# Kernel optimization log

Hardware: AMD Instinct MI355X
Metric: run time of the kernel (lower is better)

The kernel has to match this reference:

```python
import jax, jax.numpy as jnp
import numpy as np

RATIO, NH, NG, KS, RF, UP = 4, 2, 2, 3, 11.0, 2


def _cln(t, g, b):
    # channel-wise LayerNorm on NCHW (LayerNormProxy), eps=1e-5
    mu = t.mean(axis=1, keepdims=True)
    var = ((t - mu) ** 2).mean(axis=1, keepdims=True)
    return (t - mu) * jax.lax.rsqrt(var + 1e-5) * g[None, :, None, None] + b[None, :, None, None]


def _resize_ac(img, oH, oW):
    # bilinear resize, align_corners=True (F.interpolate)
    H, W = img.shape[-2], img.shape[-1]
    ys = jnp.arange(oH, dtype=img.dtype) * ((H - 1) / (oH - 1))
    y0 = jnp.clip(jnp.floor(ys), 0, H - 2).astype(jnp.int32)
    wy = ys - y0.astype(img.dtype)
    xs = jnp.arange(oW, dtype=img.dtype) * ((W - 1) / (oW - 1))
    x0 = jnp.clip(jnp.floor(xs), 0, W - 2).astype(jnp.int32)
    wx = xs - x0.astype(img.dtype)
    t = img[..., y0, :] * (1.0 - wy)[:, None] + img[..., y0 + 1, :] * wy[:, None]
    return t[..., x0] * (1.0 - wx) + t[..., x0 + 1] * wx


def _grid_sample(img, iy, ix):
    # bilinear grid_sample, padding_mode='zeros', align_corners=True
    # img [Bg,Cx,H,W]; iy,ix [Bg,N] unnormalized input-pixel coords
    H, W = img.shape[-2], img.shape[-1]
    def one(im, yy, xx):
        y0f, x0f = jnp.floor(yy), jnp.floor(xx)
        wy, wx = yy - y0f, xx - x0f
        y0, x0 = y0f.astype(jnp.int32), x0f.astype(jnp.int32)
        def gat(yi, xi):
            valid = ((yi >= 0) & (yi < H) & (xi >= 0) & (xi < W)).astype(im.dtype)
            return im[:, jnp.clip(yi, 0, H - 1), jnp.clip(xi, 0, W - 1)] * valid[None]
        return (gat(y0, x0) * ((1 - wy) * (1 - wx))[None]
                + gat(y0, x0 + 1) * ((1 - wy) * wx)[None]
                + gat(y0 + 1, x0) * (wy * (1 - wx))[None]
                + gat(y0 + 1, x0 + 1) * (wy * wx)[None])
    return jax.vmap(one)(img, iy, ix)


def _conv2d(x, w, groups=1):
    return jax.lax.conv_general_dilated(x, w, (1, 1), 'SAME', feature_group_count=groups,
                                        dimension_numbers=('NCHW', 'OIHW', 'NCHW'))


def _forward(x, ln_g, ln_b, Wq, Wk, dw_w, off_ln_g, off_ln_b, off_w, off_b, rpb):
    B, C, H, W = x.shape
    hidden = C // RATIO
    gc = hidden // NG
    c2 = hidden // NH          # attn_dim per head
    oH, oW = int(H * UP), int(W * UP)
    N1, n = oH * oW, KS * KS
    scale = c2 ** -0.5
    v = x
    xn = _cln(x, ln_g, ln_b)
    q = jnp.einsum('oc,bchw->bohw', Wq, xn)
    k = jnp.einsum('oc,bchw->bohw', Wk, xn)
    q = _resize_ac(q, oH, oW)                        # [B,hidden,oH,oW]
    # offset prediction
    q_off = q.reshape(B * NG, gc, oH, oW)
    t = _conv2d(q_off, dw_w, groups=gc)
    t = _cln(t, off_ln_g, off_ln_b)
    t = jax.nn.gelu(t, approximate=False)
    pred = _conv2d(t, off_w) + off_b[None, :, None, None]  # [Bg,2*ks^2,oH,oW]
    pad = (KS - 1) // 2
    rng = jnp.arange(-pad, pad + 1, dtype=x.dtype)
    base = jnp.stack(jnp.meshgrid(rng, rng, indexing='ij'), axis=-1)  # [KS,KS,2] (y,x)
    off = jnp.tanh(pred).reshape(B * NG, KS, KS, 2, oH, oW) * RF + base[None, :, :, :, None, None]
    py = off[:, :, :, 0] + jnp.arange(oH, dtype=x.dtype)[None, None, None, :, None]
    px = off[:, :, :, 1] + jnp.arange(oW, dtype=x.dtype)[None, None, None, None, :]
    # normalize over (oH-1,oW-1) then denormalize onto (H-1,W-1) input grid (align_corners)
    iy = (py * ((H - 1) / (oH - 1))).reshape(B * NG, -1)
    ix = (px * ((W - 1) / (oW - 1))).reshape(B * NG, -1)
    kg = k.reshape(B * NG, hidden // NG, H, W)
    vg = v.reshape(B * NG, C // NG, H, W)
    kf = _grid_sample(kg, iy, ix).reshape(B, NG, hidden // NG, n, oH, oW)
    vf = _grid_sample(vg, iy, ix).reshape(B, NG, C // NG, n, oH, oW)
    # -> [B, N1, n, g*c] -> [B, nh, N1, n, c]
    kf = kf.transpose(0, 4, 5, 3, 1, 2).reshape(B, N1, n, NH, hidden // NH).transpose(0, 3, 1, 2, 4)
    vf = vf.transpose(0, 4, 5, 3, 1, 2).reshape(B, N1, n, NH, C // NH).transpose(0, 3, 1, 2, 4)
    kf = kf + rpb                                     # relative position bias on K
    qh = q.reshape(B, NH, c2, N1).transpose(0, 1, 3, 2) * scale  # [B,nh,N1,c2]
    attn = jax.nn.softmax(jnp.einsum('bhnc,bhnkc->bhnk', qh, kf), axis=-1)
    out = jnp.einsum('bhnk,bhnkc->bhnc', attn, vf)    # [B,nh,N1,C/nh]
    return out.transpose(0, 1, 3, 2).reshape(B, C, oH, oW)


def setup_inputs() -> dict:
    key = jax.random.key(0)
    ks = jax.random.split(key, 8)
    B, C, H, W = 2, 256, 48, 48
    hidden = C // RATIO
    gc = hidden // NG
    c2 = hidden // NH
    f32 = jnp.float32
    return {
        'x': jax.random.normal(ks[0], (B, C, H, W), f32),
        'ln_g': jnp.ones((C,), f32),
        'ln_b': jnp.zeros((C,), f32),
        'Wq': jax.random.normal(ks[1], (hidden, C), f32) * 0.05,
        'Wk': jax.random.normal(ks[2], (hidden, C), f32) * 0.05,
        'dw_w': jax.random.normal(ks[3], (gc, 1, 3, 3), f32) * 0.1,
        'off_ln_g': jnp.ones((gc,), f32),
        'off_ln_b': jnp.zeros((gc,), f32),
        'off_w': jax.random.normal(ks[4], (2 * KS * KS, gc, 3, 3), f32) * 0.02,
        'off_b': jnp.zeros((2 * KS * KS,), f32),
        'rpb': jax.random.normal(ks[5], (1, NH, 1, KS * KS, c2), f32) * 0.02,
    }


def reference(x, ln_g, ln_b, Wq, Wk, dw_w, off_ln_g, off_ln_b, off_w, off_b, rpb):
    return _forward(x, ln_g, ln_b, Wq, Wk, dw_w, off_ln_g, off_ln_b, off_w, off_b, rpb)
```

## Files before the change

kernel.cpp:

```cpp
#include <hip/hip_runtime.h>
#include <cstdint>
#include <cmath>

#define NB 2
#define NC 256
#define HW 2304
#define HID 64
#define OH 96
#define OW 96
#define N1 9216
#define SCALE_ATTN 0.17677669529663689f
#define RESZ ((float)(47.0/95.0))

__device__ __host__ inline int ocb_of(int w) { return w < 2 ? w * 5 : 10 + (w - 2) * 4; }
__device__ __host__ inline int cnt_of(int w) { return w < 2 ? 5 : 4; }

__global__ void kA_prep(const float* __restrict__ x, const float* __restrict__ Wq,
                        const float* __restrict__ Wk, const float* __restrict__ off_w,
                        const float* __restrict__ dw_w, const float* __restrict__ off_b,
                        float* __restrict__ v_nhwc, float* __restrict__ WT4,
                        float* __restrict__ dwT, float* __restrict__ wg,
                        float* __restrict__ bsg) {
    int blk = blockIdx.x;
    if (blk < 1152) {
        int pt = blk % 72;
        int t2 = blk / 72;
        int ct = t2 & 3;
        int bg = t2 >> 2;
        int b = bg >> 1, g = bg & 1;
        __shared__ float tile[32][33];
        int tx = threadIdx.x & 31, row = threadIdx.x >> 5;
#pragma unroll
        for (int r = 0; r < 4; r++) {
            int c = ct * 32 + row + r * 8;
            tile[row + r * 8][tx] = x[((size_t)(b * 256 + g * 128 + c)) * HW + pt * 32 + tx];
        }
        __syncthreads();
#pragma unroll
        for (int r = 0; r < 4; r++) {
            int p = pt * 32 + row + r * 8;
            v_nhwc[((size_t)bg * HW + p) * 128 + ct * 32 + tx] = tile[tx][row + r * 8];
        }
    } else {
        int idx = (blk - 1152) * 256 + threadIdx.x;
        if (idx < 256 * 128) {
            int c = idx >> 7, t = idx & 127;
            float v = (t < 64) ? Wq[t * 256 + c] : Wk[(t - 64) * 256 + c];
            WT4[(((size_t)(c >> 2) * 128) + t) * 4 + (c & 3)] = v;
        } else if (idx < 256 * 128 + 288) {
            int i = idx - 256 * 128;
            int wi = i >> 5, c = i & 31;
            dwT[i] = dw_w[c * 9 + wi];
        } else if (idx < 256 * 128 + 288 + 4 * 288 * 5) {
            int i = idx - (256 * 128 + 288);
            int w = i / 1440, r = i - w * 1440;
            int kk = r / 5, j = r - kk * 5;
            wg[i] = (j < cnt_of(w)) ? off_w[(ocb_of(w) + j) * 288 + kk] : 0.f;
        } else if (idx < 256 * 128 + 288 + 4 * 288 * 5 + 20) {
            int i = idx - (256 * 128 + 288 + 4 * 288 * 5);
            int w = i / 5, j = i - w * 5;
            bsg[i] = (j < cnt_of(w)) ? off_b[ocb_of(w) + j] : 0.f;
        }
    }
}

__global__ __launch_bounds__(256) void k1_ln_qk(const float* __restrict__ v_nhwc,
                         const float* __restrict__ ln_g, const float* __restrict__ ln_b,
                         const float* __restrict__ WT4,
                         float* __restrict__ q_pix, float* __restrict__ k_nhwc) {
    int blk = blockIdx.x;
    int tid = threadIdx.x;
    int wv = tid >> 6, lane = tid & 63;
    __shared__ float xs[4][256];
    {
        int pix = blk * 4 + wv;
        int b = pix / HW, p = pix - b * HW;
        int c0 = lane * 2;
        float2 u0 = *(const float2*)(v_nhwc + (((size_t)(b * 2 + 0) * HW) + p) * 128 + c0);
        float2 u1 = *(const float2*)(v_nhwc + (((size_t)(b * 2 + 1) * HW) + p) * 128 + c0);
        float s = u0.x + u0.y + u1.x + u1.y;
#pragma unroll
        for (int off = 1; off < 64; off <<= 1) s += __shfl_xor(s, off);
        float mu = s * (1.f / 256.f);
        float d0 = u0.x - mu, d1 = u0.y - mu, d2 = u1.x - mu, d3 = u1.y - mu;
        float q = d0 * d0 + d1 * d1 + d2 * d2 + d3 * d3;
#pragma unroll
        for (int off = 1; off < 64; off <<= 1) q += __shfl_xor(q, off);
        float rs = rsqrtf(q * (1.f / 256.f) + 1e-5f);
        float2 w0, w1;
        w0.x = d0 * rs * ln_g[c0] + ln_b[c0];
        w0.y = d1 * rs * ln_g[c0 + 1] + ln_b[c0 + 1];
        w1.x = d2 * rs * ln_g[128 + c0] + ln_b[128 + c0];
        w1.y = d3 * rs * ln_g[129 + c0] + ln_b[129 + c0];
        *(float2*)&xs[wv][c0] = w0;
        *(float2*)&xs[wv][128 + c0] = w1;
    }
    __syncthreads();
    int o = tid & 127, ph = tid >> 7;
    float a0 = 0.f, a1 = 0.f;
    const float4* wp = (const float4*)WT4 + o;
    const float4* xa = (const float4*)xs[ph * 2];
    const float4* xb4 = (const float4*)xs[ph * 2 + 1];
#pragma unroll 8
    for (int c4 = 0; c4 < 64; c4++) {
        float4 w = wp[(size_t)c4 * 128];
        float4 p0 = xa[c4], p1 = xb4[c4];
        a0 += w.x * p0.x + w.y * p0.y + w.z * p0.z + w.w * p0.w;
        a1 += w.x * p1.x + w.y * p1.y + w.z * p1.z + w.w * p1.w;
    }
#pragma unroll
    for (int k = 0; k < 2; k++) {
        int pix = blk * 4 + ph * 2 + k;
        int b = pix / HW, p = pix - b * HW;
        float a = k ? a1 : a0;
        if (o < 64) {
            q_pix[(((size_t)b * HW) + p) * 64 + o] = a;
        } else {
            int t = o - 64, g = t >> 5, c32 = t & 31;
            k_nhwc[(((size_t)(b * 2 + g) * HW) + p) * 32 + c32] = a;
        }
    }
}

__global__ __launch_bounds__(256) void k34_off(const float* __restrict__ q_pix,
                                               const float* __restrict__ dwT,
                                               const float* __restrict__ og,
                                               const float* __restrict__ ob,
                                               const float* __restrict__ wg,
                                               const float* __restrict__ bsg,
                                               float* __restrict__ pred) {
    int blk = blockIdx.x;
    int bg = blk / 144, tile = blk - bg * 144;
    int ty0 = (tile / 12) * 8, tx0 = (tile % 12) * 8;
    int b = bg >> 1, g = bg & 1;
    int tid = threadIdx.x;
    __shared__ float ts[100 * 33];

    const float* qb = q_pix + ((size_t)b * HW) * 64 + g * 32;
    for (int item = tid; item < 3200; item += 256) {
        int pt = item >> 5, c = item & 31;
        int pyh = pt / 10, pxh = pt - pyh * 10;
        int hy = ty0 + pyh - 1, hx = tx0 + pxh - 1;
        bool inb = ((unsigned)hy < (unsigned)OH) && ((unsigned)hx < (unsigned)OW);
        float acc = 0.f;
        if (inb) {
#pragma unroll
            for (int dy = -1; dy <= 1; dy++) {
                int yy = hy + dy;
                if ((unsigned)yy >= (unsigned)OH) continue;
                float ysf = yy * RESZ;
                int y0 = min((int)ysf, 46);
                float wy = ysf - (float)y0;
#pragma unroll
                for (int dx = -1; dx <= 1; dx++) {
                    int xx = hx + dx;
                    if ((unsigned)xx >= (unsigned)OW) continue;
                    float xsf = xx * RESZ;
                    int x0 = min((int)xsf, 46);
                    float wx = xsf - (float)x0;
                    int i00 = (y0 * 48 + x0) * 64;
                    float q00 = qb[i00 + c], q01 = qb[i00 + 64 + c];
                    float q10 = qb[i00 + 48 * 64 + c], q11 = qb[i00 + 49 * 64 + c];
                    float qv = (q00 * (1.f - wy) + q10 * wy) * (1.f - wx)
                             + (q01 * (1.f - wy) + q11 * wy) * wx;
                    acc += qv * dwT[((dy + 1) * 3 + dx + 1) * 32 + c];
                }
            }
        }
        float s = acc;
#pragma unroll
        for (int off = 1; off < 32; off <<= 1) s += __shfl_xor(s, off);
        float mu = s * (1.f / 32.f);
        float d = acc - mu;
        float v = d * d;
#pragma unroll
        for (int off = 1; off < 32; off <<= 1) v += __shfl_xor(v, off);
        float rsv = rsqrtf(v * (1.f / 32.f) + 1e-5f);
        float t = d * rsv * og[c] + ob[c];
        float ge = 0.5f * t * (1.f + erff(t * 0.70710678118654752f));
        ts[pt * 33 + c] = inb ? ge : 0.f;
    }
    __syncthreads();

    int w = __builtin_amdgcn_readfirstlane(tid >> 6);
    int lane = tid & 63;
    int y = lane >> 3, x = lane & 7;
    int ocb = ocb_of(w), cnt = cnt_of(w);
    float acc[5];
#pragma unroll
    for (int j = 0; j < 5; j++) acc[j] = bsg[w * 5 + j];
    const float* tsb = &ts[(y * 10 + x) * 33];
    const float* wgp = wg + (size_t)w * 1440;
    const int kof[9] = {0, 33, 66, 330, 363, 396, 660, 693, 726};
    for (int ic = 0; ic < 32; ic++) {
#pragma unroll
        for (int k = 0; k < 9; k++) {
            float tv = tsb[kof[k] + ic];
            const float* wr = wgp + (ic * 9 + k) * 5;
#pragma unroll
            for (int j = 0; j < 5; j++) acc[j] += tv * wr[j];
        }
    }
    int p = (ty0 + y) * OW + tx0 + x;
    float* pp = pred + ((size_t)bg * N1 + p) * 18 + ocb;
#pragma unroll
    for (int j = 0; j < 5; j++)
        if (j < cnt) pp[j] = acc[j];
}

__global__ __launch_bounds__(256) void k5_attn(const float* __restrict__ pred,
                                               const float* __restrict__ q_pix,
                                               const float* __restrict__ k_nhwc,
                                               const float* __restrict__ v_nhwc,
                                               const float* __restrict__ rpb,
                                               float* __restrict__ out) {
    int tid = threadIdx.x;
    int wv = __builtin_amdgcn_readfirstlane(tid >> 6);
    int lane = tid & 63;
    int gp = blockIdx.x * 16;
    int bg = gp / N1, p0 = gp % N1;
    int b = bg >> 1, g = bg & 1;
    int pw = p0 + wv * 4;
    int oy = pw / OW, ox0 = pw % OW;

    __shared__ float4 wts[4][4][9];
    __shared__ int4   cof[4][4][9];
    __shared__ float  outb[4][4][128];

    if (lane < 36) {
        int px = lane / 9, j = lane % 9;
        int p = pw + px;
        int ky = j / 3, kx = j % 3;
        const float* pp = pred + ((size_t)bg * N1 + p) * 18;
        float pr0 = pp[j * 2];
        float pr1 = pp[j * 2 + 1];
        float th0 = 1.f - 2.f * __builtin_amdgcn_rcpf(__expf(2.f * pr0) + 1.f);
        float th1 = 1.f - 2.f * __builtin_amdgcn_rcpf(__expf(2.f * pr1) + 1.f);
        float py  = th0 * 11.0f + (float)(ky - 1) + (float)oy;
        float pxc = th1 * 11.0f + (float)(kx - 1) + (float)(ox0 + px);
        float iy = py * RESZ, ix = pxc * RESZ;
        float y0f = floorf(iy), x0f = floorf(ix);
        float wy = iy - y0f, wx = ix - x0f;
        int y0 = (int)y0f, x0 = (int)x0f;
        bool vy0 = (unsigned)y0 < 48u, vy1 = (unsigned)(y0 + 1) < 48u;
        bool vx0 = (unsigned)x0 < 48u, vx1 = (unsigned)(x0 + 1) < 48u;
        int y0c = min(max(y0, 0), 47), y1c = min(max(y0 + 1, 0), 47);
        int x0c = min(max(x0, 0), 47), x1c = min(max(x0 + 1, 0), 47);
        float4 w;
        w.x = (vy0 && vx0) ? (1.f - wy) * (1.f - wx) : 0.f;
        w.y = (vy0 && vx1) ? (1.f - wy) * wx : 0.f;
        w.z = (vy1 && vx0) ? wy * (1.f - wx) : 0.f;
        w.w = (vy1 && vx1) ? wy * wx : 0.f;
        wts[wv][px][j] = w;
        cof[wv][px][j] = make_int4(y0c * 48 + x0c, y0c * 48 + x1c,
                                   y1c * 48 + x0c, y1c * 48 + x1c);
    }
    __syncthreads();

    int c = lane & 31, h = lane >> 5;
    int c4 = (lane & 31) * 4;
    const float* kb = k_nhwc + (size_t)bg * HW * 32;
    const float* rb = rpb + (size_t)g * 288;
    const float* qb = q_pix + (size_t)b * HW * 64 + g * 32 + c;
    const float* vbase = v_nhwc + (size_t)bg * HW * 128;

    float ysf = oy * RESZ;
    int qy0 = min((int)ysf, 46);
    float qwy = ysf - (float)qy0;

    for (int px = 0; px < 4; px++) {
        float xsf = (ox0 + px) * RESZ;
        int qx0 = min((int)xsf, 46);
        float qwx = xsf - (float)qx0;
        int qi = (qy0 * 48 + qx0) * 64;
        float q00 = qb[qi], q01 = qb[qi + 64];
        float q10 = qb[qi + 48 * 64], q11 = qb[qi + 49 * 64];
        float qv = ((q00 * (1.f - qwy) + q10 * qwy) * (1.f - qwx)
                  + (q01 * (1.f - qwy) + q11 * qwy) * qwx) * SCALE_ATTN;

        float s[5], e[5];
#pragma unroll
        for (int jj = 0; jj < 5; jj++) {
            int j = jj * 2 + h;
            float partial = 0.f;
            if (j < 9) {
                float4 w = wts[wv][px][j];
                int4 co = cof[wv][px][j];
                float kv = w.x * kb[co.x * 32 + c] + w.y * kb[co.y * 32 + c]
                         + w.z * kb[co.z * 32 + c] + w.w * kb[co.w * 32 + c];
                partial = qv * (kv + rb[j * 32 + c]);
            }
#pragma unroll
            for (int off = 1; off < 32; off <<= 1) partial += __shfl_xor(partial, off);
            s[jj] = (j < 9) ? partial : -1e30f;
        }
        float m = s[0];
#pragma unroll
        for (int jj = 1; jj < 5; jj++) m = fmaxf(m, s[jj]);
        m = fmaxf(m, __shfl_xor(m, 32));
        float sum = 0.f;
#pragma unroll
        for (int jj = 0; jj < 5; jj++) { e[jj] = __expf(s[jj] - m); sum += e[jj]; }
        sum += __shfl_xor(sum, 32);
        float inv = __builtin_amdgcn_rcpf(sum);

        float4 acc = make_float4(0.f, 0.f, 0.f, 0.f);
#pragma unroll
        for (int jj = 0; jj < 5; jj++) {
            int j = jj * 2 + h;
            if (j < 9) {
                float pj = e[jj] * inv;
                float4 w = wts[wv][px][j];
                int4 co = cof[wv][px][j];
                float4 a0 = *(const float4*)(vbase + (size_t)co.x * 128 + c4);
                float4 a1 = *(const float4*)(vbase + (size_t)co.y * 128 + c4);
                float4 a2 = *(const float4*)(vbase + (size_t)co.z * 128 + c4);
                float4 a3 = *(const float4*)(vbase + (size_t)co.w * 128 + c4);
                float f0 = w.x * pj, f1 = w.y * pj, f2 = w.z * pj, f3 = w.w * pj;
                acc.x += f0 * a0.x + f1 * a1.x + f2 * a2.x + f3 * a3.x;
                acc.y += f0 * a0.y + f1 * a1.y + f2 * a2.y + f3 * a3.y;
                acc.z += f0 * a0.z + f1 * a1.z + f2 * a2.z + f3 * a3.z;
                acc.w += f0 * a0.w + f1 * a1.w + f2 * a2.w + f3 * a3.w;
            }
        }
        acc.x += __shfl_xor(acc.x, 32);
        acc.y += __shfl_xor(acc.y, 32);
        acc.z += __shfl_xor(acc.z, 32);
        acc.w += __shfl_xor(acc.w, 32);
        if (lane < 32) *(float4*)&outb[wv][px][c4] = acc;
    }
    __syncthreads();

    if (tid < 128) {
        int ch = tid;
        float* op = out + ((size_t)b * NC + g * 128 + ch) * N1 + p0;
#pragma unroll
        for (int w2 = 0; w2 < 4; w2++) {
            float4 v4 = make_float4(outb[w2][0][ch], outb[w2][1][ch],
                                    outb[w2][2][ch], outb[w2][3][ch]);
            *(float4*)(op + w2 * 4) = v4;
        }
    }
}

extern "C" void kernel_launch(void* const* d_in, const int* in_sizes, int n_in,
                              void* d_out, int out_size, void* d_ws, size_t ws_size,
                              hipStream_t stream) {
    const float* x      = (const float*)d_in[0];
    const float* ln_g   = (const float*)d_in[1];
    const float* ln_b   = (const float*)d_in[2];
    const float* Wq     = (const float*)d_in[3];
    const float* Wk     = (const float*)d_in[4];
    const float* dw_w   = (const float*)d_in[5];
    const float* off_g  = (const float*)d_in[6];
    const float* off_bt = (const float*)d_in[7];
    const float* off_w  = (const float*)d_in[8];
    const float* off_b  = (const float*)d_in[9];
    const float* rpb    = (const float*)d_in[10];
    float* out = (float*)d_out;

    float* ws = (float*)d_ws;
    float* v_nhwc = ws;
    float* WT4    = v_nhwc + 1179648;
    float* k_nhwc = WT4 + 32768;
    float* q_pix  = k_nhwc + 294912;
    float* pred   = q_pix + 294912;
    float* dwT    = pred + 663552;
    float* wg     = dwT + 288;
    float* bsg    = wg + 5760;

    kA_prep<<<1304, 256, 0, stream>>>(x, Wq, Wk, off_w, dw_w, off_b,
                                      v_nhwc, WT4, dwT, wg, bsg);
    k1_ln_qk<<<1152, 256, 0, stream>>>(v_nhwc, ln_g, ln_b, WT4, q_pix, k_nhwc);
    k34_off<<<576, 256, 0, stream>>>(q_pix, dwT, off_g, off_bt, wg, bsg, pred);
    k5_attn<<<2304, 256, 0, stream>>>(pred, q_pix, k_nhwc, v_nhwc, rpb, out);
}
```

Measured before the change: 185.1 us.

## Split offset kernel into depthwise-LN-GELU pass with fp16 buffer and 8-wave conv

The fused offset kernel used to recompute the depthwise conv, LayerNorm and GELU for every halo pixel of each 8x8 tile. It is now split into a per-pixel kernel that writes the activations once to an fp16 buffer, and a conv kernel that loads halo tiles from that buffer using 512 threads, so each wave handles 2-3 output channels. The attention kernel is also restructured to batch the q interpolation, score, softmax and value accumulation across its 4 pixels, which exposes more independent loads. This adds an extra launch and fp16 rounding of intermediate activations, and it raises register pressure in the attention kernel.

```diff
diff --git a/kernel.cpp b/kernel.cpp
--- a/kernel.cpp
+++ b/kernel.cpp
@@ -1,4 +1,5 @@
 #include <hip/hip_runtime.h>
+#include <hip/hip_fp16.h>
 #include <cstdint>
 #include <cmath>
 
@@ -12,15 +13,15 @@
 #define SCALE_ATTN 0.17677669529663689f
 #define RESZ ((float)(47.0/95.0))
 
-__device__ __host__ inline int ocb_of(int w) { return w < 2 ? w * 5 : 10 + (w - 2) * 4; }
-__device__ __host__ inline int cnt_of(int w) { return w < 2 ? 5 : 4; }
+__device__ __host__ inline int ocb8(int w) { return w < 2 ? 3 * w : 6 + 2 * (w - 2); }
+__device__ __host__ inline int cnt8(int w) { return w < 2 ? 3 : 2; }
 
 __global__ void kA_prep(const float* __restrict__ x, const float* __restrict__ Wq,
                         const float* __restrict__ Wk, const float* __restrict__ off_w,
                         const float* __restrict__ dw_w, const float* __restrict__ off_b,
                         float* __restrict__ v_nhwc, float* __restrict__ WT4,
-                        float* __restrict__ dwT, float* __restrict__ wg,
-                        float* __restrict__ bsg) {
+                        float* __restrict__ dwT, float* __restrict__ wg2,
+                        float* __restrict__ bsg2) {
     int blk = blockIdx.x;
     if (blk < 1152) {
         int pt = blk % 72;
@@ -43,23 +44,23 @@
         }
     } else {
         int idx = (blk - 1152) * 256 + threadIdx.x;
-        if (idx < 256 * 128) {
+        if (idx < 32768) {
             int c = idx >> 7, t = idx & 127;
             float v = (t < 64) ? Wq[t * 256 + c] : Wk[(t - 64) * 256 + c];
             WT4[(((size_t)(c >> 2) * 128) + t) * 4 + (c & 3)] = v;
-        } else if (idx < 256 * 128 + 288) {
-            int i = idx - 256 * 128;
+        } else if (idx < 32768 + 288) {
+            int i = idx - 32768;
             int wi = i >> 5, c = i & 31;
             dwT[i] = dw_w[c * 9 + wi];
-        } else if (idx < 256 * 128 + 288 + 4 * 288 * 5) {
-            int i = idx - (256 * 128 + 288);
-            int w = i / 1440, r = i - w * 1440;
-            int kk = r / 5, j = r - kk * 5;
-            wg[i] = (j < cnt_of(w)) ? off_w[(ocb_of(w) + j) * 288 + kk] : 0.f;
-        } else if (idx < 256 * 128 + 288 + 4 * 288 * 5 + 20) {
-            int i = idx - (256 * 128 + 288 + 4 * 288 * 5);
-            int w = i / 5, j = i - w * 5;
-            bsg[i] = (j < cnt_of(w)) ? off_b[ocb_of(w) + j] : 0.f;
+        } else if (idx < 32768 + 288 + 8 * 288 * 3) {
+            int i = idx - (32768 + 288);
+            int w = i / 864, r = i - w * 864;
+            int kk = r / 3, j = r - kk * 3;
+            wg2[i] = (j < cnt8(w)) ? off_w[(ocb8(w) + j) * 288 + kk] : 0.f;
+        } else if (idx < 32768 + 288 + 8 * 288 * 3 + 24) {
+            int i = idx - (32768 + 288 + 8 * 288 * 3);
+            int w = i / 3, j = i - w * 3;
+            bsg2[i] = (j < cnt8(w)) ? off_b[ocb8(w) + j] : 0.f;
         }
     }
 }
@@ -122,89 +123,107 @@
     }
 }
 
-__global__ __launch_bounds__(256) void k34_off(const float* __restrict__ q_pix,
-                                               const float* __restrict__ dwT,
-                                               const float* __restrict__ og,
-                                               const float* __restrict__ ob,
-                                               const float* __restrict__ wg,
-                                               const float* __restrict__ bsg,
+__global__ __launch_bounds__(256) void k3_t(const float* __restrict__ q_pix,
+                                            const float* __restrict__ dwT,
+                                            const float* __restrict__ og,
+                                            const float* __restrict__ ob,
+                                            __half* __restrict__ tbuf_h) {
+    int gid = blockIdx.x * 256 + threadIdx.x;
+    int c = gid & 31;
+    int p2 = gid >> 5;
+    int bg = p2 / N1, p = p2 - bg * N1;
+    int b = bg >> 1, g = bg & 1;
+    int oy = p / OW, ox = p - oy * OW;
+    const float* qb = q_pix + ((size_t)b * HW) * 64 + g * 32 + c;
+    float acc = 0.f;
+#pragma unroll
+    for (int dy = -1; dy <= 1; dy++) {
+        int yy = oy + dy;
+        if ((unsigned)yy >= (unsigned)OH) continue;
+        float ysf = yy * RESZ;
+        int y0 = min((int)ysf, 46);
+        float wy = ysf - (float)y0;
+#pragma unroll
+        for (int dx = -1; dx <= 1; dx++) {
+            int xx = ox + dx;
+            if ((unsigned)xx >= (unsigned)OW) continue;
+            float xsf = xx * RESZ;
+            int x0 = min((int)xsf, 46);
+            float wx = xsf - (float)x0;
+            int i00 = (y0 * 48 + x0) * 64;
+            float q00 = qb[i00], q01 = qb[i00 + 64];
+            float q10 = qb[i00 + 48 * 64], q11 = qb[i00 + 49 * 64];
+            float qv = (q00 * (1.f - wy) + q10 * wy) * (1.f - wx)
+                     + (q01 * (1.f - wy) + q11 * wy) * wx;
+            acc += qv * dwT[((dy + 1) * 3 + dx + 1) * 32 + c];
+        }
+    }
+    float s = acc;
+#pragma unroll
+    for (int off = 1; off < 32; off <<= 1) s += __shfl_xor(s, off);
+    float mu = s * (1.f / 32.f);
+    float d = acc - mu;
+    float v = d * d;
+#pragma unroll
+    for (int off = 1; off < 32; off <<= 1) v += __shfl_xor(v, off);
+    float rsv = rsqrtf(v * (1.f / 32.f) + 1e-5f);
+    float t = d * rsv * og[c] + ob[c];
+    float ge = 0.5f * t * (1.f + erff(t * 0.70710678118654752f));
+    tbuf_h[(size_t)p2 * 32 + c] = __float2half(ge);
+}
+
+__global__ __launch_bounds__(512) void k4_pred(const __half* __restrict__ tbuf_h,
+                                               const float* __restrict__ wg2,
+                                               const float* __restrict__ bsg2,
                                                float* __restrict__ pred) {
     int blk = blockIdx.x;
     int bg = blk / 144, tile = blk - bg * 144;
     int ty0 = (tile / 12) * 8, tx0 = (tile % 12) * 8;
-    int b = bg >> 1, g = bg & 1;
     int tid = threadIdx.x;
     __shared__ float ts[100 * 33];
 
-    const float* qb = q_pix + ((size_t)b * HW) * 64 + g * 32;
-    for (int item = tid; item < 3200; item += 256) {
-        int pt = item >> 5, c = item & 31;
-        int pyh = pt / 10, pxh = pt - pyh * 10;
-        int hy = ty0 + pyh - 1, hx = tx0 + pxh - 1;
-        bool inb = ((unsigned)hy < (unsigned)OH) && ((unsigned)hx < (unsigned)OW);
-        float acc = 0.f;
-        if (inb) {
-#pragma unroll
-            for (int dy = -1; dy <= 1; dy++) {
-                int yy = hy + dy;
-                if ((unsigned)yy >= (unsigned)OH) continue;
-                float ysf = yy * RESZ;
-                int y0 = min((int)ysf, 46);
-                float wy = ysf - (float)y0;
-#pragma unroll
-                for (int dx = -1; dx <= 1; dx++) {
-                    int xx = hx + dx;
-                    if ((unsigned)xx >= (unsigned)OW) continue;
-                    float xsf = xx * RESZ;
-                    int x0 = min((int)xsf, 46);
-                    float wx = xsf - (float)x0;
-                    int i00 = (y0 * 48 + x0) * 64;
-                    float q00 = qb[i00 + c], q01 = qb[i00 + 64 + c];
-                    float q10 = qb[i00 + 48 * 64 + c], q11 = qb[i00 + 49 * 64 + c];
-                    float qv = (q00 * (1.f - wy) + q10 * wy) * (1.f - wx)
-                             + (q01 * (1.f - wy) + q11 * wy) * wx;
-                    acc += qv * dwT[((dy + 1) * 3 + dx + 1) * 32 + c];
-                }
-            }
-        }
-        float s = acc;
-#pragma unroll
-        for (int off = 1; off < 32; off <<= 1) s += __shfl_xor(s, off);
-        float mu = s * (1.f / 32.f);
-        float d = acc - mu;
-        float v = d * d;
-#pragma unroll
-        for (int off = 1; off < 32; off <<= 1) v += __shfl_xor(v, off);
-        float rsv = rsqrtf(v * (1.f / 32.f) + 1e-5f);
-        float t = d * rsv * og[c] + ob[c];
-        float ge = 0.5f * t * (1.f + erff(t * 0.70710678118654752f));
-        ts[pt * 33 + c] = inb ? ge : 0.f;
+    const __half* tb = tbuf_h + (size_t)bg * N1 * 32;
+    for (int item = tid; item < 400; item += 512) {
+        int pt = item >> 2, qg = item & 3;
+        int hy = ty0 + pt / 10 - 1;
+        int hx = tx0 + pt % 10 - 1;
+        float4 raw = make_float4(0.f, 0.f, 0.f, 0.f);
+        if ((unsigned)hy < (unsigned)OH && (unsigned)hx < (unsigned)OW)
+            raw = *(const float4*)(tb + ((size_t)(hy * OW + hx)) * 32 + qg * 8);
+        const __half2* h2 = (const __half2*)&raw;
+        int base = pt * 33 + qg * 8;
+#pragma unroll
+        for (int i = 0; i < 4; i++) {
+            float2 f = __half22float2(h2[i]);
+            ts[base + i * 2] = f.x;
+            ts[base + i * 2 + 1] = f.y;
+        }
     }
     __syncthreads();
 
     int w = __builtin_amdgcn_readfirstlane(tid >> 6);
     int lane = tid & 63;
     int y = lane >> 3, x = lane & 7;
-    int ocb = ocb_of(w), cnt = cnt_of(w);
-    float acc[5];
-#pragma unroll
-    for (int j = 0; j < 5; j++) acc[j] = bsg[w * 5 + j];
+    int ocb = ocb8(w), cnt = cnt8(w);
+    float acc[3];
+#pragma unroll
+    for (int j = 0; j < 3; j++) acc[j] = bsg2[w * 3 + j];
     const float* tsb = &ts[(y * 10 + x) * 33];
-    const float* wgp = wg + (size_t)w * 1440;
+    const float* wgp = wg2 + (size_t)w * 864;
     const int kof[9] = {0, 33, 66, 330, 363, 396, 660, 693, 726};
     for (int ic = 0; ic < 32; ic++) {
 #pragma unroll
         for (int k = 0; k < 9; k++) {
             float tv = tsb[kof[k] + ic];
-            const float* wr = wgp + (ic * 9 + k) * 5;
-#pragma unroll
-            for (int j = 0; j < 5; j++) acc[j] += tv * wr[j];
+            const float* wr = wgp + (ic * 9 + k) * 3;
+#pragma unroll
+            for (int j = 0; j < 3; j++) acc[j] += tv * wr[j];
         }
     }
     int p = (ty0 + y) * OW + tx0 + x;
     float* pp = pred + ((size_t)bg * N1 + p) * 18 + ocb;
 #pragma unroll
-    for (int j = 0; j < 5; j++)
+    for (int j = 0; j < 3; j++)
         if (j < cnt) pp[j] = acc[j];
 }
 
@@ -268,6 +287,15 @@
     int qy0 = min((int)ysf, 46);
     float qwy = ysf - (float)qy0;
 
+    float rv[5];
+#pragma unroll
+    for (int jj = 0; jj < 5; jj++) {
+        int j = jj * 2 + h;
+        rv[jj] = (j < 9) ? rb[j * 32 + c] : 0.f;
+    }
+
+    float qv[4];
+#pragma unroll
     for (int px = 0; px < 4; px++) {
         float xsf = (ox0 + px) * RESZ;
         int qx0 = min((int)xsf, 46);
@@ -275,10 +303,13 @@
         int qi = (qy0 * 48 + qx0) * 64;
         float q00 = qb[qi], q01 = qb[qi + 64];
         float q10 = qb[qi + 48 * 64], q11 = qb[qi + 49 * 64];
-        float qv = ((q00 * (1.f - qwy) + q10 * qwy) * (1.f - qwx)
-                  + (q01 * (1.f - qwy) + q11 * qwy) * qwx) * SCALE_ATTN;
-
-        float s[5], e[5];
+        qv[px] = ((q00 * (1.f - qwy) + q10 * qwy) * (1.f - qwx)
+                + (q01 * (1.f - qwy) + q11 * qwy) * qwx) * SCALE_ATTN;
+    }
+
+    float s[4][5];
+#pragma unroll
+    for (int px = 0; px < 4; px++) {
 #pragma unroll
         for (int jj = 0; jj < 5; jj++) {
             int j = jj * 2 + h;
@@ -288,28 +319,40 @@
                 int4 co = cof[wv][px][j];
                 float kv = w.x * kb[co.x * 32 + c] + w.y * kb[co.y * 32 + c]
                          + w.z * kb[co.z * 32 + c] + w.w * kb[co.w * 32 + c];
-                partial = qv * (kv + rb[j * 32 + c]);
+                partial = qv[px] * (kv + rv[jj]);
             }
 #pragma unroll
             for (int off = 1; off < 32; off <<= 1) partial += __shfl_xor(partial, off);
-            s[jj] = (j < 9) ? partial : -1e30f;
-        }
-        float m = s[0];
-#pragma unroll
-        for (int jj = 1; jj < 5; jj++) m = fmaxf(m, s[jj]);
+            s[px][jj] = (j < 9) ? partial : -1e30f;
+        }
+    }
+
+#pragma unroll
+    for (int px = 0; px < 4; px++) {
+        float m = s[px][0];
+#pragma unroll
+        for (int jj = 1; jj < 5; jj++) m = fmaxf(m, s[px][jj]);
         m = fmaxf(m, __shfl_xor(m, 32));
+        float e[5];
         float sum = 0.f;
 #pragma unroll
-        for (int jj = 0; jj < 5; jj++) { e[jj] = __expf(s[jj] - m); sum += e[jj]; }
+        for (int jj = 0; jj < 5; jj++) { e[jj] = __expf(s[px][jj] - m); sum += e[jj]; }
         sum += __shfl_xor(sum, 32);
         float inv = __builtin_amdgcn_rcpf(sum);
-
-        float4 acc = make_float4(0.f, 0.f, 0.f, 0.f);
+#pragma unroll
+        for (int jj = 0; jj < 5; jj++) s[px][jj] = e[jj] * inv;
+    }
+
+    float4 acc[4];
+#pragma unroll
+    for (int px = 0; px < 4; px++) acc[px] = make_float4(0.f, 0.f, 0.f, 0.f);
+#pragma unroll
+    for (int px = 0; px < 4; px++) {
 #pragma unroll
         for (int jj = 0; jj < 5; jj++) {
             int j = jj * 2 + h;
             if (j < 9) {
-                float pj = e[jj] * inv;
+                float pj = s[px][jj];
                 float4 w = wts[wv][px][j];
                 int4 co = cof[wv][px][j];
                 float4 a0 = *(const float4*)(vbase + (size_t)co.x * 128 + c4);
@@ -317,17 +360,20 @@
                 float4 a2 = *(const float4*)(vbase + (size_t)co.z * 128 + c4);
                 float4 a3 = *(const float4*)(vbase + (size_t)co.w * 128 + c4);
                 float f0 = w.x * pj, f1 = w.y * pj, f2 = w.z * pj, f3 = w.w * pj;
-                acc.x += f0 * a0.x + f1 * a1.x + f2 * a2.x + f3 * a3.x;
-                acc.y += f0 * a0.y + f1 * a1.y + f2 * a2.y + f3 * a3.y;
-                acc.z += f0 * a0.z + f1 * a1.z + f2 * a2.z + f3 * a3.z;
-                acc.w += f0 * a0.w + f1 * a1.w + f2 * a2.w + f3 * a3.w;
+                acc[px].x += f0 * a0.x + f1 * a1.x + f2 * a2.x + f3 * a3.x;
+                acc[px].y += f0 * a0.y + f1 * a1.y + f2 * a2.y + f3 * a3.y;
+                acc[px].z += f0 * a0.z + f1 * a1.z + f2 * a2.z + f3 * a3.z;
+                acc[px].w += f0 * a0.w + f1 * a1.w + f2 * a2.w + f3 * a3.w;
             }
         }
-        acc.x += __shfl_xor(acc.x, 32);
-        acc.y += __shfl_xor(acc.y, 32);
-        acc.z += __shfl_xor(acc.z, 32);
-        acc.w += __shfl_xor(acc.w, 32);
-        if (lane < 32) *(float4*)&outb[wv][px][c4] = acc;
+    }
+#pragma unroll
+    for (int px = 0; px < 4; px++) {
+        acc[px].x += __shfl_xor(acc[px].x, 32);
+        acc[px].y += __shfl_xor(acc[px].y, 32);
+        acc[px].z += __shfl_xor(acc[px].z, 32);
+        acc[px].w += __shfl_xor(acc[px].w, 32);
+        if (lane < 32) *(float4*)&outb[wv][px][c4] = acc[px];
     }
     __syncthreads();
 
@@ -366,12 +412,14 @@
     float* q_pix  = k_nhwc + 294912;
     float* pred   = q_pix + 294912;
     float* dwT    = pred + 663552;
-    float* wg     = dwT + 288;
-    float* bsg    = wg + 5760;
-
-    kA_prep<<<1304, 256, 0, stream>>>(x, Wq, Wk, off_w, dw_w, off_b,
-                                      v_nhwc, WT4, dwT, wg, bsg);
+    float* wg2    = dwT + 288;
+    float* bsg2   = wg2 + 6912;
+    __half* tbuf_h = (__half*)(bsg2 + 24);
+
+    kA_prep<<<1309, 256, 0, stream>>>(x, Wq, Wk, off_w, dw_w, off_b,
+                                      v_nhwc, WT4, dwT, wg2, bsg2);
     k1_ln_qk<<<1152, 256, 0, stream>>>(v_nhwc, ln_g, ln_b, WT4, q_pix, k_nhwc);
-    k34_off<<<576, 256, 0, stream>>>(q_pix, dwT, off_g, off_bt, wg, bsg, pred);
+    k3_t<<<4608, 256, 0, stream>>>(q_pix, dwT, off_g, off_bt, tbuf_h);
+    k4_pred<<<576, 512, 0, stream>>>(tbuf_h, wg2, bsg2, pred);
     k5_attn<<<2304, 256, 0, stream>>>(pred, q_pix, k_nhwc, v_nhwc, rpb, out);
 }
```

Result: faster. 166.7 us (-9.9%).
